# Kernel tuning notes

Measured on AMD Instinct MI355X. Metric: run time of the kernel, lower is better.

Reference implementation:

```python
import jax, jax.numpy as jnp
import numpy as np

N, E, NG = 8192, 65536, 8
EMB, SH = 32, 9
HID = EMB * SH
SDIM, M, KV = 16, 2048, 16  # M = master_rate*N masters (static top-k); KV virtual nbrs/node
RMAX, NB, PC = 10.0, 8, 5
MLPD, MSH, NL = 64, 32, 3
NEMB = 10


def _radial(r):
    # r: [E,1] -> Bessel basis * polynomial cutoff envelope, [E, NB]
    x = r / RMAX
    n = jnp.arange(1, NB + 1, dtype=r.dtype)
    bes = jnp.sqrt(2.0 / RMAX) * jnp.sin(n * jnp.pi * x) / jnp.maximum(r, 1e-9)
    p = float(PC)
    env = (1.0 - (p + 1) * (p + 2) / 2 * x ** PC + p * (p + 2) * x ** (PC + 1)
           - p * (p + 1) / 2 * x ** (PC + 2))
    env = jnp.where(x < 1.0, env, 0.0)
    return bes * env


def _sph(vec):
    # component-normalized real spherical harmonics l=0,1,2 of normalized vec
    r = jnp.linalg.norm(vec, axis=-1, keepdims=True)
    u = vec / jnp.maximum(r, 1e-9)
    x, y, z = u[..., 0], u[..., 1], u[..., 2]
    s3, s5, s15 = jnp.sqrt(3.0), jnp.sqrt(5.0), jnp.sqrt(15.0)
    Y = jnp.stack([
        jnp.ones_like(x),
        s3 * y, s3 * z, s3 * x,
        s15 * x * y, s15 * y * z, 0.5 * s5 * (3 * z * z - 1.0),
        s15 * x * z, 0.5 * s15 * (x * x - y * y)], axis=-1)
    return Y, r


def _conv(h, src, dst, sh, ef, W, rw1, rb1, rw2, rb2, valid, nnodes):
    # TFN-style conv: per-edge radial MLP -> per-sh-path weights, tensor product, scatter-sum
    rad = jax.nn.relu(ef @ rw1 + rb1) @ rw2 + rb2  # [E, SH]
    coeff = sh * rad                               # [E, SH]
    h_src = h[src]                                 # gather [E, in]
    out = W.shape[-1]
    msg = jnp.zeros((src.shape[0], out), h.dtype)
    for s in range(SH):  # small fixed loop over sh paths (avoids [E,in*SH] blowup)
        msg = msg + coeff[:, s:s + 1] * (h_src @ W[:, s, :])
    if valid is not None:
        msg = msg * valid[:, None]
    return jnp.zeros((nnodes, out), h.dtype).at[dst].add(msg)


def _scatter_softmax(sc, idx, nseg):
    mx = jax.ops.segment_max(sc, idx, nseg)
    e = jnp.exp(sc - mx[idx])
    s = jax.ops.segment_sum(e, idx, nseg)
    return e / (s[idx] + 1e-9)


def _forward(atoms, pos, edge_index, batch_ids, emb_table, W0, W12,
             rw1, rb1, rw2, rb2, msw1, msb1, msw2, msb2,
             vq, vk, aw1, ab1, aw2, ab2, pw1, pb1, pw2, pb2):
    h = emb_table[atoms]
    src, dst = edge_index[0], edge_index[1]
    for i in range(NL):
        W = W0 if i == 0 else W12[i - 1]
        # ---- local message passing over original edges ----
        vec = pos[src] - pos[dst]
        sh, r = _sph(vec)
        ef = _radial(r)
        h_up = _conv(h, src, dst, sh, ef, W, rw1[i], rb1[i], rw2[i], rb2[i], None, N)
        h_local = h_up.at[:, :h.shape[-1]].add(h)  # h_update + right-pad(h)
        # ---- master selection (static top-k of soft scores, k = master_rate*N) ----
        hs = h_local[:, :SDIM]
        m = jax.nn.sigmoid((jax.nn.relu(hs @ msw1[i] + msb1[i]) @ msw2[i] + msb2[i])[:, 0])
        _, midx = jax.lax.top_k(m, M)
        midx = jnp.sort(midx)
        inv = jnp.full((N,), -1, jnp.int32).at[midx].set(jnp.arange(M, dtype=jnp.int32))
        ms, md = inv[src], inv[dst]
        vi = (ms >= 0) & (md >= 0)           # induced-subgraph edge mask
        msc = jnp.where(vi, ms, 0)
        mdc = jnp.where(vi, md, 0)
        vif = vi.astype(h.dtype)
        h_m = h_local[midx]
        pos_m = pos[midx]
        hms = h_m[:, :SDIM]
        # induced dense adjacency over masters
        adj = jnp.minimum(jnp.zeros((M, M), h.dtype).at[msc, mdc].add(vif), 1.0)
        # ---- virtual edge generation (attention over masters) ----
        S = (hms @ vq[i]) @ (hms @ vk[i]).T / jnp.sqrt(jnp.asarray(SDIM, h.dtype))
        blocked = jnp.eye(M, dtype=bool) | (adj > 0)
        S = jnp.where(blocked, -jnp.inf, S)
        A_virtual = jax.nn.softmax(S, axis=-1)
        _, tk = jax.lax.top_k(S, KV)          # top-KV virtual nbrs per master (static)
        row = jnp.repeat(jnp.arange(M), KV)
        col = tk.reshape(-1)
        sv = jnp.concatenate([row, col])      # undirected virtual edges
        dv = jnp.concatenate([col, row])
        # ---- master-level edges: induced (masked) + virtual ----
        srcm = jnp.concatenate([msc, sv])
        dstm = jnp.concatenate([mdc, dv])
        vecm = pos_m[srcm] - pos_m[dstm]
        shm, rm = _sph(vecm)
        efm = _radial(rm)
        # scatter-softmax attention weights on virtual edges
        att_in = jnp.concatenate([hms[sv], hms[dv], efm[E:]], axis=-1)
        sc = (jax.nn.relu(att_in @ aw1[i] + ab1[i]) @ aw2[i] + ab2[i])[:, 0]
        wv = _scatter_softmax(sc, dv, M)
        full_w = jnp.concatenate([vif, wv])   # induced edges weight 1 (0 if invalid)
        efm = efm * full_w[:, None]
        if i == 0:
            h_hier = h_m  # first layer: in_irreps != out_irreps -> skip master conv
        else:
            validm = jnp.concatenate([vif, jnp.ones_like(wv)])
            h_mu = _conv(h_m, srcm, dstm, shm, efm, W,
                         rw1[i], rb1[i], rw2[i], rb2[i], validm, M)
            h_hier = h_mu + h_m
        # ---- scatter masters back, soft mix ----
        h_exp = jnp.zeros_like(h_local).at[midx].set(h_hier)
        me = m[:, None]
        h = (1.0 - me) * h_local + me * h_exp
    pooled = jax.ops.segment_sum(h[:, :EMB], batch_ids, NG)  # global_add_pool
    return jax.nn.relu(pooled @ pw1 + pb1) @ pw2 + pb2


def setup_inputs() -> dict:
    key = jax.random.key(0)
    ks = jax.random.split(key, 30)
    g = lambda k, shape, s=0.1: jax.random.normal(k, shape, jnp.float32) * s
    return dict(
        atoms=jax.random.randint(ks[0], (N,), 0, NEMB),
        pos=jax.random.normal(ks[1], (N, 3), jnp.float32) * 3.0,
        edge_index=jax.random.randint(ks[2], (2, E), 0, N),
        batch_ids=jnp.sort(jax.random.randint(ks[3], (N,), 0, NG)),
        emb_table=g(ks[4], (NEMB, EMB), 1.0),
        W0=g(ks[5], (EMB, SH, HID)),
        W12=g(ks[6], (NL - 1, HID, SH, HID), 0.05),
        rw1=g(ks[7], (NL, NB, MLPD), 0.3), rb1=g(ks[8], (NL, MLPD)),
        rw2=g(ks[9], (NL, MLPD, SH), 0.3), rb2=g(ks[10], (NL, SH)),
        msw1=g(ks[11], (NL, SDIM, MSH), 0.3), msb1=g(ks[12], (NL, MSH)),
        msw2=g(ks[13], (NL, MSH, 1), 0.3), msb2=g(ks[14], (NL, 1)),
        vq=g(ks[15], (NL, SDIM, SDIM), 0.3), vk=g(ks[16], (NL, SDIM, SDIM), 0.3),
        aw1=g(ks[17], (NL, 2 * SDIM + NB, SDIM), 0.3), ab1=g(ks[18], (NL, SDIM)),
        aw2=g(ks[19], (NL, SDIM, 1), 0.3), ab2=g(ks[20], (NL, 1)),
        pw1=g(ks[21], (EMB, EMB), 0.3), pb1=g(ks[22], (EMB,)),
        pw2=g(ks[23], (EMB, 1), 0.3), pb2=g(ks[24], (1,)),
    )


def reference(atoms, pos, edge_index, batch_ids, emb_table, W0, W12,
              rw1, rb1, rw2, rb2, msw1, msb1, msw2, msb2,
              vq, vk, aw1, ab1, aw2, ab2, pw1, pb1, pw2, pb2):
    return _forward(atoms, pos, edge_index, batch_ids, emb_table, W0, W12,
                    rw1, rb1, rw2, rb2, msw1, msb1, msw2, msb2,
                    vq, vk, aw1, ab1, aw2, ab2, pw1, pb1, pw2, pb2)
```

## Files before the change

### kernel.cpp

```cpp
#include <hip/hip_runtime.h>
#include <math.h>

#define NN     8192
#define EE     65536
#define NGR    8
#define EMBD   32
#define NSH    9
#define HIDD   288
#define SD     16
#define MM     2048
#define KVK    16
#define NBAS   8
#define MLPDIM 64
#define MSHD   32
#define MK     (MM*KVK)
#define EH     (EE + 2*MK)

typedef __attribute__((ext_vector_type(8))) short bf16x8;
typedef __attribute__((ext_vector_type(4))) float f32x4;

static __device__ __forceinline__ float relu_(float x) { return fmaxf(x, 0.f); }

__device__ __forceinline__ unsigned short f2b(float f) {
  unsigned int u = __float_as_uint(f);
  unsigned int r = (u + 0x7FFFu + ((u >> 16) & 1u)) >> 16;
  return (unsigned short)r;
}
__device__ __forceinline__ float b2f(unsigned short h) {
  return __uint_as_float(((unsigned int)h) << 16);
}

__device__ __forceinline__ void radial8(float r, float ef[8]) {
  float x = r * 0.1f;
  float invr = 1.0f / fmaxf(r, 1e-9f);
  float env = 0.0f;
  if (x < 1.0f) {
    float x2 = x * x, x4 = x2 * x2, x5 = x4 * x;
    env = 1.0f - 21.0f * x5 + 35.0f * x5 * x - 15.0f * x5 * x2;
  }
  const float cst = 0.4472135954999579f;
  float a = 3.14159265358979323846f * x;
#pragma unroll
  for (int n = 1; n <= NBAS; ++n)
    ef[n - 1] = cst * sinf((float)n * a) * invr * env;
}

__device__ __forceinline__ void sph9(float vx, float vy, float vz, float Y[9], float& r) {
  r = sqrtf(vx * vx + vy * vy + vz * vz);
  float inv = 1.0f / fmaxf(r, 1e-9f);
  float x = vx * inv, y = vy * inv, z = vz * inv;
  const float s3 = 1.7320508075688772f, s5 = 2.23606797749979f, s15 = 3.872983346207417f;
  Y[0] = 1.0f;
  Y[1] = s3 * y; Y[2] = s3 * z; Y[3] = s3 * x;
  Y[4] = s15 * x * y; Y[5] = s15 * y * z;
  Y[6] = 0.5f * s5 * (3.0f * z * z - 1.0f);
  Y[7] = s15 * x * z;
  Y[8] = 0.5f * s15 * (x * x - y * y);
}

__device__ __forceinline__ void radmlp(const float ef[8], const float* w1, const float* b1,
                                       const float* w2, const float* b2, float rad[9]) {
  float z[MLPDIM];
#pragma unroll
  for (int d = 0; d < MLPDIM; ++d) {
    float a = b1[d];
#pragma unroll
    for (int b = 0; b < NBAS; ++b) a += ef[b] * w1[b * MLPDIM + d];
    z[d] = relu_(a);
  }
#pragma unroll
  for (int s = 0; s < 9; ++s) {
    float a = b2[s];
#pragma unroll
    for (int d = 0; d < MLPDIM; ++d) a += z[d] * w2[d * 9 + s];
    rad[s] = a;
  }
}

__device__ __forceinline__ unsigned int fkey(float f) {
  unsigned int u = __float_as_uint(f);
  return (u & 0x80000000u) ? ~u : (u | 0x80000000u);
}
__device__ __forceinline__ float funkey(unsigned int k) {
  unsigned int u = (k & 0x80000000u) ? (k ^ 0x80000000u) : ~k;
  return __uint_as_float(u);
}

__device__ __forceinline__ void svdv(int j, const int* __restrict__ tkb, int& s, int& d) {
  if (j < MK) { s = j / KVK; d = tkb[j]; }
  else        { int t = j - MK; s = tkb[t]; d = t / KVK; }
}
__device__ __forceinline__ int dvof(int j, const int* __restrict__ tkb) {
  return (j < MK) ? tkb[j] : (j - MK) / KVK;
}


__global__ void k_init_h(const int* __restrict__ atoms, const float* __restrict__ emb,
                         float* __restrict__ hA) {
  int t = blockIdx.x * 256 + threadIdx.x;
  int n = t / HIDD, c = t - n * HIDD;
  hA[t] = (c < EMBD) ? emb[atoms[n] * EMBD + c] : 0.0f;
}

__global__ void k_geom(const float* __restrict__ pos, const int* __restrict__ ei,
                       float* __restrict__ sh_e, float* __restrict__ ef_e) {
  int e = blockIdx.x * 256 + threadIdx.x;
  int s = ei[e], d = ei[EE + e];
  float vx = pos[s * 3] - pos[d * 3];
  float vy = pos[s * 3 + 1] - pos[d * 3 + 1];
  float vz = pos[s * 3 + 2] - pos[d * 3 + 2];
  float Y[9], r;
  sph9(vx, vy, vz, Y, r);
  float ef[8]; radial8(r, ef);
#pragma unroll
  for (int t = 0; t < 9; ++t) sh_e[e * 9 + t] = Y[t];
#pragma unroll
  for (int b = 0; b < 8; ++b) ef_e[e * 8 + b] = ef[b];
}

__global__ __launch_bounds__(256) void k_radcoeff(const float* __restrict__ ef_e,
    const float* __restrict__ sh_e, const float* __restrict__ rw1, const float* __restrict__ rb1,
    const float* __restrict__ rw2, const float* __restrict__ rb2, float* __restrict__ coeff) {
  __shared__ float w1[NBAS * MLPDIM], b1[MLPDIM], w2[MLPDIM * 9], b2[9];
  int tid = threadIdx.x;
  for (int t = tid; t < NBAS * MLPDIM; t += 256) w1[t] = rw1[t];
  for (int t = tid; t < MLPDIM * 9; t += 256) w2[t] = rw2[t];
  if (tid < MLPDIM) b1[tid] = rb1[tid];
  if (tid < 9) b2[tid] = rb2[tid];
  __syncthreads();
  int e = blockIdx.x * 256 + tid;
  float ef[8];
#pragma unroll
  for (int b = 0; b < 8; ++b) ef[b] = ef_e[e * 8 + b];
  float rad[9]; radmlp(ef, w1, b1, w2, b2, rad);
#pragma unroll
  for (int s = 0; s < 9; ++s) coeff[(size_t)e * 9 + s] = sh_e[e * 9 + s] * rad[s];
}

__global__ __launch_bounds__(256) void k_wt(const float* __restrict__ W, int K,
                                            unsigned short* __restrict__ Whi,
                                            unsigned short* __restrict__ Wlo) {
  __shared__ unsigned short Th[32][290];
  __shared__ unsigned short Tl[32][290];
  int k0 = blockIdx.x * 32;
  int tid = threadIdx.x;
  for (int t = tid; t < 32 * 288; t += 256) {
    int kk = t / 288, o = t % 288;
    float wv = W[(size_t)(k0 + kk) * 288 + o];
    unsigned short hi = f2b(wv);
    Th[kk][o] = hi;
    Tl[kk][o] = f2b(wv - b2f(hi));
  }
  __syncthreads();
  for (int o = tid; o < 288; o += 256) {
    unsigned short th[32], tl[32];
#pragma unroll
    for (int kk = 0; kk < 32; ++kk) { th[kk] = Th[kk][o]; tl[kk] = Tl[kk][o]; }
#pragma unroll
    for (int q = 0; q < 4; ++q) {
      *(float4*)&Whi[(size_t)o * K + k0 + 8 * q] = *(float4*)&th[8 * q];
      *(float4*)&Wlo[(size_t)o * K + k0 + 8 * q] = *(float4*)&tl[8 * q];
    }
  }
}

__global__ void k_hist(const int* __restrict__ didx, int n, int* __restrict__ cnt) {
  int e = blockIdx.x * 256 + threadIdx.x;
  if (e >= n) return;
  int d = didx[e];
  if (d >= 0) atomicAdd(&cnt[d], 1);
}
__global__ __launch_bounds__(256) void k_scan(const int* __restrict__ cnt, int* __restrict__ off,
                                              int* __restrict__ cur, int nb) {
  __shared__ int ps[257];
  int tid = threadIdx.x;
  int chunk = nb / 256;
  int s = 0;
  for (int i = 0; i < chunk; ++i) s += cnt[tid * chunk + i];
  __shared__ int part[256];
  part[tid] = s;
  __syncthreads();
  if (tid == 0) {
    int a = 0;
    for (int i = 0; i < 256; ++i) { ps[i] = a; a += part[i]; }
    ps[256] = a;
  }
  __syncthreads();
  int a = ps[tid];
  for (int i = 0; i < chunk; ++i) {
    int idx = tid * chunk + i;
    off[idx] = a; cur[idx] = a;
    a += cnt[idx];
  }
  if (tid == 255) off[nb] = a;
}
__global__ void k_scat(const int* __restrict__ didx, int n, int* __restrict__ cur,
                       int* __restrict__ elist) {
  int e = blockIdx.x * 256 + threadIdx.x;
  if (e >= n) return;
  int d = didx[e];
  if (d < 0) return;
  int pos = atomicAdd(&cur[d], 1);
  elist[pos] = e;
}

template <int NJ>
__global__ __launch_bounds__(256) void k_gatherBbf(const float* __restrict__ h,
    const float* __restrict__ coeff, const int* __restrict__ sidx,
    const int* __restrict__ elist, const int* __restrict__ off,
    unsigned short* __restrict__ Ghi, unsigned short* __restrict__ Glo) {
  constexpr int INW = (NJ == 1) ? 32 : 288;
  constexpr int KG = INW * 9;
  __shared__ float red[3][64][NJ * 9];
  int w = threadIdx.x >> 6, l = threadIdx.x & 63;
  int d = blockIdx.x;
  int e0 = off[d], e1 = off[d + 1];
  float acc[NJ][9];
#pragma unroll
  for (int j = 0; j < NJ; ++j)
#pragma unroll
    for (int s = 0; s < 9; ++s) acc[j][s] = 0.f;
  for (int p = e0 + w; p < e1; p += 4) {
    int e = elist[p];
    int src = sidx[e];
    const float* hr = h + (size_t)src * HIDD;
    float hv[NJ];
#pragma unroll
    for (int j = 0; j < NJ; ++j)
      hv[j] = (l + 64 * j < INW) ? hr[l + 64 * j] : 0.f;
    const float* cfp = coeff + (size_t)e * 9;
    float cf[9];
#pragma unroll
    for (int s = 0; s < 9; ++s) cf[s] = cfp[s];
#pragma unroll
    for (int j = 0; j < NJ; ++j)
#pragma unroll
      for (int s = 0; s < 9; ++s) acc[j][s] += hv[j] * cf[s];
  }
  if (w > 0) {
#pragma unroll
    for (int j = 0; j < NJ; ++j)
#pragma unroll
      for (int s = 0; s < 9; ++s) red[w - 1][l][j * 9 + s] = acc[j][s];
  }
  __syncthreads();
  if (w == 0) {
    unsigned short* Gdh = Ghi + (size_t)d * KG;
    unsigned short* Gdl = Glo + (size_t)d * KG;
#pragma unroll
    for (int j = 0; j < NJ; ++j) {
      int k = l + 64 * j;
      if (k < INW) {
#pragma unroll
        for (int s = 0; s < 9; ++s) {
          float v = acc[j][s] + red[0][l][j * 9 + s] + red[1][l][j * 9 + s] +
                    red[2][l][j * 9 + s];
          unsigned short hi = f2b(v);
          Gdh[k * 9 + s] = hi;
          Gdl[k * 9 + s] = f2b(v - b2f(hi));
        }
      }
    }
  }
}

__global__ __launch_bounds__(256) void k_gatherBf(const float* __restrict__ h,
    const float* __restrict__ coeff, const int* __restrict__ sidx,
    const int* __restrict__ elist, const int* __restrict__ off, float* __restrict__ Gf) {
  constexpr int NJ = 5, INW = 288, KG = 2592, NW = 16;
  __shared__ float red[3][64][NJ * 9];
  int w = threadIdx.x >> 6, l = threadIdx.x & 63;
  int d = blockIdx.x, q = blockIdx.y;
  int e0 = off[d], e1 = off[d + 1];
  float acc[NJ][9];
#pragma unroll
  for (int j = 0; j < NJ; ++j)
#pragma unroll
    for (int s = 0; s < 9; ++s) acc[j][s] = 0.f;
  for (int p = e0 + q * 4 + w; p < e1; p += NW) {
    int e = elist[p];
    int src = sidx[e];
    const float* hr = h + (size_t)src * HIDD;
    float hv[NJ];
#pragma unroll
    for (int j = 0; j < NJ; ++j)
      hv[j] = (l + 64 * j < INW) ? hr[l + 64 * j] : 0.f;
    const float* cfp = coeff + (size_t)e * 9;
    float cf[9];
#pragma unroll
    for (int s = 0; s < 9; ++s) cf[s] = cfp[s];
#pragma unroll
    for (int j = 0; j < NJ; ++j)
#pragma unroll
      for (int s = 0; s < 9; ++s) acc[j][s] += hv[j] * cf[s];
  }
  if (w > 0) {
#pragma unroll
    for (int j = 0; j < NJ; ++j)
#pragma unroll
      for (int s = 0; s < 9; ++s) red[w - 1][l][j * 9 + s] = acc[j][s];
  }
  __syncthreads();
  if (w == 0) {
    float* Gd = Gf + ((size_t)q * gridDim.x + d) * KG;
#pragma unroll
    for (int j = 0; j < NJ; ++j) {
      int k = l + 64 * j;
      if (k < INW) {
#pragma unroll
        for (int s = 0; s < 9; ++s)
          Gd[k * 9 + s] = acc[j][s] + red[0][l][j * 9 + s] + red[1][l][j * 9 + s] +
                          red[2][l][j * 9 + s];
      }
    }
  }
}

__global__ void k_redG(const float* __restrict__ Gf, unsigned short* __restrict__ Ghi,
                       unsigned short* __restrict__ Glo) {
  const size_t PS = (size_t)MM * 2592;
  size_t t = (size_t)blockIdx.x * 256 + threadIdx.x;
  float v = Gf[t] + Gf[PS + t] + Gf[2 * PS + t] + Gf[3 * PS + t];
  unsigned short hi = f2b(v);
  Ghi[t] = hi;
  Glo[t] = f2b(v - b2f(hi));
}

template <int KK>
__global__ __launch_bounds__(256) void k_mgemm3(const unsigned short* __restrict__ Ahi,
    const unsigned short* __restrict__ Alo,
    const unsigned short* __restrict__ Whi, const unsigned short* __restrict__ Wlo,
    float* __restrict__ Cpart) {
  constexpr int slabs = KK / 32;
  __shared__ unsigned short Bh[144 * 40];
  __shared__ unsigned short Bl[144 * 40];
  int m0 = blockIdx.x * 64, cb = blockIdx.y * 144;
  int M = gridDim.x * 64;
  int Z = gridDim.z, z = blockIdx.z;
  int s0 = (z * slabs) / Z, s1 = ((z + 1) * slabs) / Z;
  float* C = Cpart + (size_t)z * M * 288;
  int tid = threadIdx.x;
  int w = tid >> 6, l = tid & 63;
  int lr = l & 15, oct = l >> 4;
  int arow = m0 + 16 * w + lr;
  f32x4 acc[9];
#pragma unroll
  for (int t = 0; t < 9; ++t) acc[t] = (f32x4){0.f, 0.f, 0.f, 0.f};
  for (int sl = s0; sl < s1; ++sl) {
    int k0 = sl * 32;
    __syncthreads();
    for (int t = tid; t < 1152; t += 256) {
      int hsel = t / 576;
      int qq = t - hsel * 576;
      int c = qq >> 2, ko = qq & 3;
      const unsigned short* Wsrc = hsel ? Wlo : Whi;
      float4 v = *(const float4*)&Wsrc[(size_t)(cb + c) * KK + k0 + ko * 8];
      unsigned short* Bdst = hsel ? Bl : Bh;
      *(float4*)&Bdst[c * 40 + ko * 8] = v;
    }
    __syncthreads();
    bf16x8 ah = *(const bf16x8*)&Ahi[(size_t)arow * KK + k0 + oct * 8];
    bf16x8 al = *(const bf16x8*)&Alo[(size_t)arow * KK + k0 + oct * 8];
#pragma unroll
    for (int t = 0; t < 9; ++t) {
      bf16x8 bh = *(const bf16x8*)&Bh[(16 * t + lr) * 40 + oct * 8];
      bf16x8 bl = *(const bf16x8*)&Bl[(16 * t + lr) * 40 + oct * 8];
      acc[t] = __builtin_amdgcn_mfma_f32_16x16x32_bf16(ah, bh, acc[t], 0, 0, 0);
      acc[t] = __builtin_amdgcn_mfma_f32_16x16x32_bf16(ah, bl, acc[t], 0, 0, 0);
      acc[t] = __builtin_amdgcn_mfma_f32_16x16x32_bf16(al, bh, acc[t], 0, 0, 0);
    }
  }
#pragma unroll
  for (int t = 0; t < 9; ++t) {
#pragma unroll
    for (int r = 0; r < 4; ++r)
      C[(size_t)(m0 + 16 * w + 4 * oct + r) * 288 + cb + 16 * t + lr] = acc[t][r];
  }
}

template <int Z>
__global__ void k_redN(const float* __restrict__ part, const float* __restrict__ hA,
                       float* __restrict__ hB, int INL) {
  int t = blockIdx.x * 256 + threadIdx.x;
  float v = 0.f;
#pragma unroll
  for (int z = 0; z < Z; ++z) v += part[(size_t)z * NN * 288 + t];
  int c = t % 288;
  if (c < INL) v += hA[t];
  hB[t] = v;
}
template <int Z>
__global__ void k_redH(const float* __restrict__ part, const float* __restrict__ hM,
                       float* __restrict__ hMu) {
  int t = blockIdx.x * 256 + threadIdx.x;
  float v = hM[t];
#pragma unroll
  for (int z = 0; z < Z; ++z) v += part[(size_t)z * MM * 288 + t];
  hMu[t] = v;
}

__global__ __launch_bounds__(256) void k_mmlp(const float* __restrict__ hB,
    const float* __restrict__ msw1, const float* __restrict__ msb1,
    const float* __restrict__ msw2, const float* __restrict__ msb2, float* __restrict__ mbuf) {
  __shared__ float w1[SD * MSHD], b1[MSHD], w2[MSHD];
  __shared__ float b2s;
  int tid = threadIdx.x;
  for (int t = tid; t < SD * MSHD; t += 256) w1[t] = msw1[t];
  if (tid < MSHD) { b1[tid] = msb1[tid]; w2[tid] = msw2[tid]; }
  if (tid == 0) b2s = msb2[0];
  __syncthreads();
  int n = blockIdx.x * 256 + tid;
  float hs[SD];
#pragma unroll
  for (int k = 0; k < SD; ++k) hs[k] = hB[(size_t)n * HIDD + k];
  float acc = b2s;
#pragma unroll
  for (int d = 0; d < MSHD; ++d) {
    float a = b1[d];
#pragma unroll
    for (int k = 0; k < SD; ++k) a += hs[k] * w1[k * MSHD + d];
    acc += relu_(a) * w2[d];
  }
  mbuf[n] = 1.0f / (1.0f + expf(-acc));
}

__global__ __launch_bounds__(256) void k_rank2(const float* __restrict__ mbuf,
                                               int* __restrict__ rankb) {
  __shared__ float vj[1024];
  __shared__ float vi_s[64];
  __shared__ int part[4][64];
  int tid = threadIdx.x;
  int i0 = blockIdx.x * 64, j0 = blockIdx.y * 1024;
  for (int t = tid; t < 1024; t += 256) vj[t] = mbuf[j0 + t];
  if (tid < 64) vi_s[tid] = mbuf[i0 + tid];
  __syncthreads();
  int il = tid & 63, js = tid >> 6;
  int i = i0 + il;
  float v = vi_s[il];
  int cnt = 0;
#pragma unroll 8
  for (int jj = js * 256; jj < js * 256 + 256; ++jj) {
    float w = vj[jj];
    cnt += (int)((w > v) | ((w == v) & (j0 + jj < i)));
  }
  part[js][il] = cnt;
  __syncthreads();
  if (tid < 64) {
    int c = part[0][tid] + part[1][tid] + part[2][tid] + part[3][tid];
    atomicAdd(&rankb[i0 + tid], c);
  }
}

__global__ __launch_bounds__(256) void k_select2(const int* __restrict__ rankb,
                                                 int* __restrict__ inv, int* __restrict__ midx) {
  __shared__ int part[256], ps[256];
  int tid = threadIdx.x;
  const int CH = NN / 256;
  int base = tid * CH;
  unsigned int mask = 0;
  int s = 0;
#pragma unroll
  for (int i = 0; i < CH; ++i) {
    int sel = (rankb[base + i] < MM) ? 1 : 0;
    mask |= (unsigned int)sel << i;
    s += sel;
  }
  part[tid] = s;
  __syncthreads();
  if (tid == 0) {
    int a = 0;
    for (int i = 0; i < 256; ++i) { ps[i] = a; a += part[i]; }
  }
  __syncthreads();
  int pos = ps[tid];
#pragma unroll
  for (int i = 0; i < CH; ++i) {
    if ((mask >> i) & 1u) {
      inv[base + i] = pos;
      midx[pos] = base + i;
      ++pos;
    } else {
      inv[base + i] = -1;
    }
  }
}

__global__ void k_gather_hm(const float* __restrict__ hB, const int* __restrict__ midx,
                            const float* __restrict__ pos, float* __restrict__ hM,
                            float* __restrict__ posm) {
  int t = blockIdx.x * 256 + threadIdx.x;
  int j = t / HIDD, c = t - j * HIDD;
  int n = midx[j];
  hM[t] = hB[(size_t)n * HIDD + c];
  if (c < 3) posm[j * 3 + c] = pos[n * 3 + c];
}

__global__ void k_qk(const float* __restrict__ hM, const float* __restrict__ vq,
                     const float* __restrict__ vk, float* __restrict__ qb, float* __restrict__ kb) {
  int g = blockIdx.x * 256 + threadIdx.x;
  int j = g >> 5, c = g & 31;
  const float* w = (c < 16) ? vq : vk;
  int cc = c & 15;
  float a = 0.f;
#pragma unroll
  for (int k = 0; k < SD; ++k) a += hM[(size_t)j * HIDD + k] * w[k * SD + cc];
  if (c < 16) qb[j * SD + cc] = a; else kb[j * SD + cc] = a;
}

__global__ __launch_bounds__(256) void k_S(const float* __restrict__ qb,
                                           const float* __restrict__ kb, float* __restrict__ S) {
  __shared__ float qs[64][17], ks[64][17];
  int r0 = blockIdx.y * 64, c0 = blockIdx.x * 64;
  int tid = threadIdx.x;
  for (int t = tid; t < 64 * 16; t += 256) {
    qs[t / 16][t % 16] = qb[(size_t)(r0 + t / 16) * SD + t % 16];
    ks[t / 16][t % 16] = kb[(size_t)(c0 + t / 16) * SD + t % 16];
  }
  __syncthreads();
  int tx = tid & 15, ty = tid >> 4;
  float acc[4][4] = {};
#pragma unroll
  for (int k = 0; k < 16; ++k) {
    float a[4], b[4];
#pragma unroll
    for (int i = 0; i < 4; ++i) a[i] = qs[ty * 4 + i][k];
#pragma unroll
    for (int j = 0; j < 4; ++j) b[j] = ks[tx * 4 + j][k];
#pragma unroll
    for (int i = 0; i < 4; ++i)
#pragma unroll
      for (int j = 0; j < 4; ++j) acc[i][j] += a[i] * b[j];
  }
#pragma unroll
  for (int i = 0; i < 4; ++i)
#pragma unroll
    for (int j = 0; j < 4; ++j) {
      int r = r0 + ty * 4 + i, c = c0 + tx * 4 + j;
      S[(size_t)r * MM + c] = (r == c) ? -INFINITY : acc[i][j] * 0.25f;
    }
}

__global__ void k_adj(const int* __restrict__ ei, const int* __restrict__ inv,
                      float* __restrict__ S) {
  int e = blockIdx.x * 256 + threadIdx.x;
  int ms = inv[ei[e]], md = inv[ei[EE + e]];
  if (ms >= 0 && md >= 0) S[(size_t)ms * MM + md] = -INFINITY;
}

__global__ __launch_bounds__(64) void k_topkv(const float* __restrict__ S, int* __restrict__ tkb) {
  int row = blockIdx.x;
  int lane = threadIdx.x;
  const float* Sr = S + (size_t)row * MM;
  float v[32];
#pragma unroll
  for (int t = 0; t < 32; ++t) v[t] = Sr[lane + 64 * t];
  unsigned int selmask = 0;
  for (int it = 0; it < KVK; ++it) {
    float best = -INFINITY;
    int bcol = 0x7fffffff;
#pragma unroll
    for (int t = 0; t < 32; ++t) {
      if (!((selmask >> t) & 1u)) {
        int c = lane + 64 * t;
        float val = v[t];
        if (val > best || (val == best && c < bcol)) { best = val; bcol = c; }
      }
    }
#pragma unroll
    for (int off = 1; off < 64; off <<= 1) {
      float ov = __shfl_xor(best, off);
      int oc = __shfl_xor(bcol, off);
      if (ov > best || (ov == best && oc < bcol)) { best = ov; bcol = oc; }
    }
    if (lane == (bcol & 63)) selmask |= 1u << (bcol >> 6);
    if (lane == 0) tkb[row * KVK + it] = bcol;
  }
}

__global__ __launch_bounds__(256) void k_att(const float* __restrict__ hM,
    const float* __restrict__ posm, const int* __restrict__ tkb,
    const float* __restrict__ aw1, const float* __restrict__ ab1,
    const float* __restrict__ aw2, const float* __restrict__ ab2, float* __restrict__ scb) {
  __shared__ float w1[40 * SD], b1[SD], w2[SD];
  __shared__ float b2s;
  int tid = threadIdx.x;
  for (int t = tid; t < 40 * SD; t += 256) w1[t] = aw1[t];
  if (tid < SD) { b1[tid] = ab1[tid]; w2[tid] = aw2[tid]; }
  if (tid == 0) b2s = ab2[0];
  __syncthreads();
  int j = blockIdx.x * 256 + tid;
  int s, d; svdv(j, tkb, s, d);
  float vx = posm[s * 3] - posm[d * 3];
  float vy = posm[s * 3 + 1] - posm[d * 3 + 1];
  float vz = posm[s * 3 + 2] - posm[d * 3 + 2];
  float r = sqrtf(vx * vx + vy * vy + vz * vz);
  float ef[8]; radial8(r, ef);
  float hsv[SD], hdv[SD];
#pragma unroll
  for (int k = 0; k < SD; ++k) { hsv[k] = hM[(size_t)s * HIDD + k]; hdv[k] = hM[(size_t)d * HIDD + k]; }
  float acc = b2s;
#pragma unroll
  for (int o = 0; o < SD; ++o) {
    float a = b1[o];
#pragma unroll
    for (int k = 0; k < SD; ++k) a += hsv[k] * w1[k * SD + o];
#pragma unroll
    for (int k = 0; k < SD; ++k) a += hdv[k] * w1[(SD + k) * SD + o];
#pragma unroll
    for (int b = 0; b < 8; ++b) a += ef[b] * w1[(2 * SD + b) * SD + o];
    acc += relu_(a) * w2[o];
  }
  scb[j] = acc;
}

__global__ void k_segmax(const float* __restrict__ scb, const int* __restrict__ tkb,
                         unsigned int* __restrict__ segmax) {
  int j = blockIdx.x * 256 + threadIdx.x;
  atomicMax(&segmax[dvof(j, tkb)], fkey(scb[j]));
}
__global__ void k_segexp(const float* __restrict__ scb, const int* __restrict__ tkb,
                         const unsigned int* __restrict__ segmax, float* __restrict__ segsum,
                         float* __restrict__ wvb) {
  int j = blockIdx.x * 256 + threadIdx.x;
  int d = dvof(j, tkb);
  float e = expf(scb[j] - funkey(segmax[d]));
  wvb[j] = e;
  atomicAdd(&segsum[d], e);
}

__global__ void k_hier_first(const int* __restrict__ ei, const int* __restrict__ inv,
                             int* __restrict__ sb, int* __restrict__ db) {
  int e = blockIdx.x * 256 + threadIdx.x;
  int ms = inv[ei[e]], md = inv[ei[EE + e]];
  bool val = (ms >= 0) && (md >= 0);
  sb[e] = val ? ms : 0;
  db[e] = val ? md : -1;
}

__global__ __launch_bounds__(256) void k_coeff_virt(const float* __restrict__ posm,
    const int* __restrict__ tkb, const float* __restrict__ wvb,
    const float* __restrict__ segsum,
    const float* __restrict__ rw1, const float* __restrict__ rb1,
    const float* __restrict__ rw2, const float* __restrict__ rb2,
    float* __restrict__ coeff, int* __restrict__ sb, int* __restrict__ db) {
  __shared__ float w1[NBAS * MLPDIM], b1[MLPDIM], w2[MLPDIM * 9], b2[9];
  int tid = threadIdx.x;
  for (int t = tid; t < NBAS * MLPDIM; t += 256) w1[t] = rw1[t];
  for (int t = tid; t < MLPDIM * 9; t += 256) w2[t] = rw2[t];
  if (tid < MLPDIM) b1[tid] = rb1[tid];
  if (tid < 9) b2[tid] = rb2[tid];
  __syncthreads();
  int j = blockIdx.x * 256 + tid;
  int s, d; svdv(j, tkb, s, d);
  float vx = posm[s * 3] - posm[d * 3];
  float vy = posm[s * 3 + 1] - posm[d * 3 + 1];
  float vz = posm[s * 3 + 2] - posm[d * 3 + 2];
  float Y[9], r;
  sph9(vx, vy, vz, Y, r);
  float ef[8]; radial8(r, ef);
  float w = wvb[j] / (segsum[d] + 1e-9f);
#pragma unroll
  for (int b = 0; b < 8; ++b) ef[b] *= w;
  float rad[9]; radmlp(ef, w1, b1, w2, b2, rad);
  int e = EE + j;
#pragma unroll
  for (int t = 0; t < 9; ++t) coeff[(size_t)e * 9 + t] = Y[t] * rad[t];
  sb[e] = s;
  db[e] = d;
}

__global__ void k_combine(const float* __restrict__ hB, const float* __restrict__ hier,
                          const float* __restrict__ mbuf, const int* __restrict__ inv,
                          float* __restrict__ hA) {
  int t = blockIdx.x * 256 + threadIdx.x;
  int n = t / HIDD;
  float f = mbuf[n];
  float v = (1.0f - f) * hB[t];
  int j = inv[n];
  if (j >= 0) v += f * hier[(size_t)j * HIDD + (t - n * HIDD)];
  hA[t] = v;
}

__global__ void k_pool(const float* __restrict__ hA, const int* __restrict__ bids,
                       float* __restrict__ pooled) {
  int t = blockIdx.x * 256 + threadIdx.x;
  int n = t / EMBD, c = t - n * EMBD;
  atomicAdd(&pooled[bids[n] * EMBD + c], hA[(size_t)n * HIDD + c]);
}

__global__ void k_head(const float* __restrict__ pooled, const float* __restrict__ pw1,
                       const float* __restrict__ pb1, const float* __restrict__ pw2,
                       const float* __restrict__ pb2, float* __restrict__ out) {
  __shared__ float z[NGR][EMBD];
  int tid = threadIdx.x;
  int g = tid / EMBD, c2 = tid % EMBD;
  if (g < NGR) {
    float a = pb1[c2];
    for (int c = 0; c < EMBD; ++c) a += pooled[g * EMBD + c] * pw1[c * EMBD + c2];
    z[g][c2] = relu_(a);
  }
  __syncthreads();
  if (tid < NGR) {
    float a = pb2[0];
    for (int c = 0; c < EMBD; ++c) a += z[tid][c] * pw2[c];
    out[tid] = a;
  }
}


extern "C" void kernel_launch(void* const* d_in, const int* in_sizes, int n_in,
                              void* d_out, int out_size, void* d_ws, size_t ws_size,
                              hipStream_t stream) {
  const int* atoms = (const int*)d_in[0];
  const float* pos = (const float*)d_in[1];
  const int* ei = (const int*)d_in[2];
  const int* bids = (const int*)d_in[3];
  const float* emb = (const float*)d_in[4];
  const float* W0 = (const float*)d_in[5];
  const float* W12 = (const float*)d_in[6];
  const float* rw1 = (const float*)d_in[7];
  const float* rb1 = (const float*)d_in[8];
  const float* rw2 = (const float*)d_in[9];
  const float* rb2 = (const float*)d_in[10];
  const float* msw1 = (const float*)d_in[11];
  const float* msb1 = (const float*)d_in[12];
  const float* msw2 = (const float*)d_in[13];
  const float* msb2 = (const float*)d_in[14];
  const float* vq = (const float*)d_in[15];
  const float* vk = (const float*)d_in[16];
  const float* aw1 = (const float*)d_in[17];
  const float* ab1 = (const float*)d_in[18];
  const float* aw2 = (const float*)d_in[19];
  const float* ab2 = (const float*)d_in[20];
  const float* pw1 = (const float*)d_in[21];
  const float* pb1 = (const float*)d_in[22];
  const float* pw2 = (const float*)d_in[23];
  const float* pb2 = (const float*)d_in[24];
  float* out = (float*)d_out;

  char* p = (char*)d_ws;
  auto alloc = [&](size_t n) { char* r = p; p += (n + 255) & ~(size_t)255; return r; };
  float* hA = (float*)alloc((size_t)NN * HIDD * 4);
  float* hB = (float*)alloc((size_t)NN * HIDD * 4);
  float* hM = (float*)alloc((size_t)MM * HIDD * 4);
  float* hMu = (float*)alloc((size_t)MM * HIDD * 4);
  float* S = (float*)alloc((size_t)MM * MM * 4);
  float* sh_e = (float*)alloc((size_t)EE * 9 * 4);
  float* ef_e = (float*)alloc((size_t)EE * 8 * 4);
  float* coeff = (float*)alloc((size_t)EH * 9 * 4);
  float* mbuf = (float*)alloc((size_t)NN * 4);
  int* rankb = (int*)alloc((size_t)NN * 4);
  int* inv = (int*)alloc((size_t)NN * 4);
  int* midx = (int*)alloc((size_t)MM * 4);
  float* posm = (float*)alloc((size_t)MM * 3 * 4);
  float* qb = (float*)alloc((size_t)MM * SD * 4);
  float* kb = (float*)alloc((size_t)MM * SD * 4);
  int* tkb = (int*)alloc((size_t)MM * KVK * 4);
  float* scb = (float*)alloc((size_t)2 * MK * 4);
  float* wvb = (float*)alloc((size_t)2 * MK * 4);
  unsigned int* segmax = (unsigned int*)alloc((size_t)MM * 4);
  float* segsum = (float*)alloc((size_t)MM * 4);
  int* sb = (int*)alloc((size_t)EH * 4);
  int* db = (int*)alloc((size_t)EH * 4);
  float* pooled = (float*)alloc((size_t)NGR * EMBD * 4);
  char* Gblk = alloc((size_t)NN * 2592 * 4);
  unsigned short* Ghi = (unsigned short*)Gblk;
  unsigned short* Glo = Ghi + (size_t)NN * 2592;
  float* Gf = (float*)Gblk;
  unsigned short* Ghhi = (unsigned short*)alloc((size_t)MM * 2592 * 2);
  unsigned short* Ghlo = (unsigned short*)alloc((size_t)MM * 2592 * 2);
  unsigned short* Wh0 = (unsigned short*)alloc((size_t)288 * 288 * 2);
  unsigned short* Wl0 = (unsigned short*)alloc((size_t)288 * 288 * 2);
  unsigned short* Wh1 = (unsigned short*)alloc((size_t)2592 * 288 * 2);
  unsigned short* Wl1 = (unsigned short*)alloc((size_t)2592 * 288 * 2);
  unsigned short* Wh2 = (unsigned short*)alloc((size_t)2592 * 288 * 2);
  unsigned short* Wl2 = (unsigned short*)alloc((size_t)2592 * 288 * 2);
  float* Cpart = (float*)alloc((size_t)4 * NN * 288 * 4);
  int* cntN = (int*)alloc((size_t)NN * 4);
  int* offN = (int*)alloc((size_t)(NN + 1) * 4);
  int* curN = (int*)alloc((size_t)NN * 4);
  int* elN = (int*)alloc((size_t)EE * 4);
  int* cntH = (int*)alloc((size_t)MM * 4);
  int* offH = (int*)alloc((size_t)(MM + 1) * 4);
  int* curH = (int*)alloc((size_t)MM * 4);
  int* elH = (int*)alloc((size_t)EH * 4);

  const int* srcI = ei;
  const int* dstI = ei + EE;

  k_init_h<<<NN * HIDD / 256, 256, 0, stream>>>(atoms, emb, hA);
  k_geom<<<EE / 256, 256, 0, stream>>>(pos, ei, sh_e, ef_e);

  k_wt<<<288 / 32, 256, 0, stream>>>(W0, 288, Wh0, Wl0);
  k_wt<<<2592 / 32, 256, 0, stream>>>(W12, 2592, Wh1, Wl1);
  k_wt<<<2592 / 32, 256, 0, stream>>>(W12 + (size_t)2592 * 288, 2592, Wh2, Wl2);

  hipMemsetAsync(cntN, 0, NN * 4, stream);
  k_hist<<<EE / 256, 256, 0, stream>>>(dstI, EE, cntN);
  k_scan<<<1, 256, 0, stream>>>(cntN, offN, curN, NN);
  k_scat<<<EE / 256, 256, 0, stream>>>(dstI, EE, curN, elN);

  for (int L = 0; L < 3; ++L) {
    const unsigned short* Wh = (L == 0) ? Wh0 : ((L == 1) ? Wh1 : Wh2);
    const unsigned short* Wl = (L == 0) ? Wl0 : ((L == 1) ? Wl1 : Wl2);
    const float* lrw1 = rw1 + L * NBAS * MLPDIM;
    const float* lrb1 = rb1 + L * MLPDIM;
    const float* lrw2 = rw2 + L * MLPDIM * 9;
    const float* lrb2 = rb2 + L * 9;

    k_radcoeff<<<EE / 256, 256, 0, stream>>>(ef_e, sh_e, lrw1, lrb1, lrw2, lrb2, coeff);
    if (L == 0) {
      k_gatherBbf<1><<<NN, 256, 0, stream>>>(hA, coeff, srcI, elN, offN, Ghi, Glo);
      k_mgemm3<288><<<dim3(NN / 64, 2, 2), 256, 0, stream>>>(Ghi, Glo, Wh, Wl, Cpart);
      k_redN<2><<<NN * 288 / 256, 256, 0, stream>>>(Cpart, hA, hB, EMBD);
    } else {
      k_gatherBbf<5><<<NN, 256, 0, stream>>>(hA, coeff, srcI, elN, offN, Ghi, Glo);
      k_mgemm3<2592><<<dim3(NN / 64, 2, 4), 256, 0, stream>>>(Ghi, Glo, Wh, Wl, Cpart);
      k_redN<4><<<NN * 288 / 256, 256, 0, stream>>>(Cpart, hA, hB, HIDD);
    }
    k_mmlp<<<NN / 256, 256, 0, stream>>>(hB, msw1 + L * SD * MSHD, msb1 + L * MSHD,
                                         msw2 + L * MSHD, msb2 + L, mbuf);
    hipMemsetAsync(rankb, 0, NN * 4, stream);
    k_rank2<<<dim3(NN / 64, 8), 256, 0, stream>>>(mbuf, rankb);
    k_select2<<<1, 256, 0, stream>>>(rankb, inv, midx);
    k_gather_hm<<<MM * HIDD / 256, 256, 0, stream>>>(hB, midx, pos, hM, posm);

    if (L > 0) {
      k_qk<<<MM * 32 / 256, 256, 0, stream>>>(hM, vq + L * SD * SD, vk + L * SD * SD, qb, kb);
      k_S<<<dim3(MM / 64, MM / 64), 256, 0, stream>>>(qb, kb, S);
      k_adj<<<EE / 256, 256, 0, stream>>>(ei, inv, S);
      k_topkv<<<MM, 64, 0, stream>>>(S, tkb);
      k_att<<<2 * MK / 256, 256, 0, stream>>>(hM, posm, tkb, aw1 + L * 40 * SD, ab1 + L * SD,
                                              aw2 + L * SD, ab2 + L, scb);
      hipMemsetAsync(segmax, 0, MM * 4, stream);
      hipMemsetAsync(segsum, 0, MM * 4, stream);
      k_segmax<<<2 * MK / 256, 256, 0, stream>>>(scb, tkb, segmax);
      k_segexp<<<2 * MK / 256, 256, 0, stream>>>(scb, tkb, segmax, segsum, wvb);
      k_hier_first<<<EE / 256, 256, 0, stream>>>(ei, inv, sb, db);
      k_coeff_virt<<<2 * MK / 256, 256, 0, stream>>>(posm, tkb, wvb, segsum,
                                                     lrw1, lrb1, lrw2, lrb2, coeff, sb, db);
      hipMemsetAsync(cntH, 0, MM * 4, stream);
      k_hist<<<EH / 256, 256, 0, stream>>>(db, EH, cntH);
      k_scan<<<1, 256, 0, stream>>>(cntH, offH, curH, MM);
      k_scat<<<EH / 256, 256, 0, stream>>>(db, EH, curH, elH);
      k_gatherBf<<<dim3(MM, 4), 256, 0, stream>>>(hM, coeff, sb, elH, offH, Gf);
      k_redG<<<MM * 2592 / 256, 256, 0, stream>>>(Gf, Ghhi, Ghlo);
      k_mgemm3<2592><<<dim3(MM / 64, 2, 8), 256, 0, stream>>>(Ghhi, Ghlo, Wh, Wl, Cpart);
      k_redH<8><<<MM * 288 / 256, 256, 0, stream>>>(Cpart, hM, hMu);
    }
    const float* hier = (L == 0) ? hM : hMu;
    k_combine<<<NN * HIDD / 256, 256, 0, stream>>>(hB, hier, mbuf, inv, hA);
  }

  hipMemsetAsync(pooled, 0, (size_t)NGR * EMBD * 4, stream);
  k_pool<<<NN * EMBD / 256, 256, 0, stream>>>(hA, bids, pooled);
  k_head<<<1, 256, 0, stream>>>(pooled, pw1, pb1, pw2, pb2, out);
}
```

Before: 1.290 ms.

## Precompute sorted edge sources, coalesce gather writeback, drop rank atomics and memsets

Edge scatter now also writes each sorted edge's source index. The gather kernels read it directly instead of chasing elist then sidx, and they process two edges per iteration. Gather results are first reduced into shared memory, then written by all 256 threads in a contiguous, coalesced pattern instead of strided writes from a single wave. Ranking writes per-slice partial counts to an 8x buffer that select sums, which removes the atomics and the memset. The attention kernel loads node features as float4, and the two segment memsets are merged into one, which assumes segmax and segsum sit next to each other in memory.

```diff
diff --git a/kernel.cpp b/kernel.cpp
--- a/kernel.cpp
+++ b/kernel.cpp
@@ -194,20 +194,21 @@
   }
   if (tid == 255) off[nb] = a;
 }
-__global__ void k_scat(const int* __restrict__ didx, int n, int* __restrict__ cur,
-                       int* __restrict__ elist) {
+__global__ void k_scat(const int* __restrict__ didx, const int* __restrict__ sidx, int n,
+                       int* __restrict__ cur, int* __restrict__ elist, int* __restrict__ esrc) {
   int e = blockIdx.x * 256 + threadIdx.x;
   if (e >= n) return;
   int d = didx[e];
   if (d < 0) return;
   int pos = atomicAdd(&cur[d], 1);
   elist[pos] = e;
+  esrc[pos] = sidx[e];
 }
 
 template <int NJ>
 __global__ __launch_bounds__(256) void k_gatherBbf(const float* __restrict__ h,
-    const float* __restrict__ coeff, const int* __restrict__ sidx,
-    const int* __restrict__ elist, const int* __restrict__ off,
+    const float* __restrict__ coeff, const int* __restrict__ elist,
+    const int* __restrict__ esrc, const int* __restrict__ off,
     unsigned short* __restrict__ Ghi, unsigned short* __restrict__ Glo) {
   constexpr int INW = (NJ == 1) ? 32 : 288;
   constexpr int KG = INW * 9;
@@ -220,9 +221,9 @@
   for (int j = 0; j < NJ; ++j)
 #pragma unroll
     for (int s = 0; s < 9; ++s) acc[j][s] = 0.f;
-  for (int p = e0 + w; p < e1; p += 4) {
+  auto edge = [&](int p) {
     int e = elist[p];
-    int src = sidx[e];
+    int src = esrc[p];
     const float* hr = h + (size_t)src * HIDD;
     float hv[NJ];
 #pragma unroll
@@ -236,7 +237,10 @@
     for (int j = 0; j < NJ; ++j)
 #pragma unroll
       for (int s = 0; s < 9; ++s) acc[j][s] += hv[j] * cf[s];
-  }
+  };
+  int p = e0 + w;
+  for (; p + 4 < e1; p += 8) { edge(p); edge(p + 4); }
+  if (p < e1) edge(p);
   if (w > 0) {
 #pragma unroll
     for (int j = 0; j < NJ; ++j)
@@ -245,28 +249,29 @@
   }
   __syncthreads();
   if (w == 0) {
-    unsigned short* Gdh = Ghi + (size_t)d * KG;
-    unsigned short* Gdl = Glo + (size_t)d * KG;
-#pragma unroll
-    for (int j = 0; j < NJ; ++j) {
-      int k = l + 64 * j;
-      if (k < INW) {
-#pragma unroll
-        for (int s = 0; s < 9; ++s) {
-          float v = acc[j][s] + red[0][l][j * 9 + s] + red[1][l][j * 9 + s] +
-                    red[2][l][j * 9 + s];
-          unsigned short hi = f2b(v);
-          Gdh[k * 9 + s] = hi;
-          Gdl[k * 9 + s] = f2b(v - b2f(hi));
-        }
+#pragma unroll
+    for (int j = 0; j < NJ; ++j)
+#pragma unroll
+      for (int s = 0; s < 9; ++s) {
+        int idx = j * 9 + s;
+        red[0][l][idx] = acc[j][s] + red[0][l][idx] + red[1][l][idx] + red[2][l][idx];
       }
-    }
+  }
+  __syncthreads();
+  unsigned short* Gdh = Ghi + (size_t)d * KG;
+  unsigned short* Gdl = Glo + (size_t)d * KG;
+  for (int i = threadIdx.x; i < KG; i += 256) {
+    int k = i / 9, s = i - 9 * k;
+    float v = red[0][k & 63][(k >> 6) * 9 + s];
+    unsigned short hi = f2b(v);
+    Gdh[i] = hi;
+    Gdl[i] = f2b(v - b2f(hi));
   }
 }
 
 __global__ __launch_bounds__(256) void k_gatherBf(const float* __restrict__ h,
-    const float* __restrict__ coeff, const int* __restrict__ sidx,
-    const int* __restrict__ elist, const int* __restrict__ off, float* __restrict__ Gf) {
+    const float* __restrict__ coeff, const int* __restrict__ elist,
+    const int* __restrict__ esrc, const int* __restrict__ off, float* __restrict__ Gf) {
   constexpr int NJ = 5, INW = 288, KG = 2592, NW = 16;
   __shared__ float red[3][64][NJ * 9];
   int w = threadIdx.x >> 6, l = threadIdx.x & 63;
@@ -277,14 +282,15 @@
   for (int j = 0; j < NJ; ++j)
 #pragma unroll
     for (int s = 0; s < 9; ++s) acc[j][s] = 0.f;
-  for (int p = e0 + q * 4 + w; p < e1; p += NW) {
+  auto edge = [&](int p) {
     int e = elist[p];
-    int src = sidx[e];
+    int src = esrc[p];
     const float* hr = h + (size_t)src * HIDD;
     float hv[NJ];
 #pragma unroll
     for (int j = 0; j < NJ; ++j)
-      hv[j] = (l + 64 * j < INW) ? hr[l + 64 * j] : 0.f;
+      hv[j] = hr[l + 64 * j < INW ? l + 64 * j : 0];
+    if (l + 256 >= INW) hv[4] = 0.f;
     const float* cfp = coeff + (size_t)e * 9;
     float cf[9];
 #pragma unroll
@@ -293,7 +299,10 @@
     for (int j = 0; j < NJ; ++j)
 #pragma unroll
       for (int s = 0; s < 9; ++s) acc[j][s] += hv[j] * cf[s];
-  }
+  };
+  int p = e0 + q * 4 + w;
+  for (; p + NW < e1; p += 2 * NW) { edge(p); edge(p + NW); }
+  if (p < e1) edge(p);
   if (w > 0) {
 #pragma unroll
     for (int j = 0; j < NJ; ++j)
@@ -302,17 +311,19 @@
   }
   __syncthreads();
   if (w == 0) {
-    float* Gd = Gf + ((size_t)q * gridDim.x + d) * KG;
-#pragma unroll
-    for (int j = 0; j < NJ; ++j) {
-      int k = l + 64 * j;
-      if (k < INW) {
-#pragma unroll
-        for (int s = 0; s < 9; ++s)
-          Gd[k * 9 + s] = acc[j][s] + red[0][l][j * 9 + s] + red[1][l][j * 9 + s] +
-                          red[2][l][j * 9 + s];
+#pragma unroll
+    for (int j = 0; j < NJ; ++j)
+#pragma unroll
+      for (int s = 0; s < 9; ++s) {
+        int idx = j * 9 + s;
+        red[0][l][idx] = acc[j][s] + red[0][l][idx] + red[1][l][idx] + red[2][l][idx];
       }
-    }
+  }
+  __syncthreads();
+  float* Gd = Gf + ((size_t)q * gridDim.x + d) * KG;
+  for (int i = threadIdx.x; i < KG; i += 256) {
+    int k = i / 9, s = i - 9 * k;
+    Gd[i] = red[0][k & 63][(k >> 6) * 9 + s];
   }
 }
 
@@ -425,7 +436,7 @@
 }
 
 __global__ __launch_bounds__(256) void k_rank2(const float* __restrict__ mbuf,
-                                               int* __restrict__ rankb) {
+                                               int* __restrict__ rank8) {
   __shared__ float vj[1024];
   __shared__ float vi_s[64];
   __shared__ int part[4][64];
@@ -447,11 +458,11 @@
   __syncthreads();
   if (tid < 64) {
     int c = part[0][tid] + part[1][tid] + part[2][tid] + part[3][tid];
-    atomicAdd(&rankb[i0 + tid], c);
-  }
-}
-
-__global__ __launch_bounds__(256) void k_select2(const int* __restrict__ rankb,
+    rank8[(size_t)blockIdx.y * NN + i0 + tid] = c;
+  }
+}
+
+__global__ __launch_bounds__(256) void k_select2(const int* __restrict__ rank8,
                                                  int* __restrict__ inv, int* __restrict__ midx) {
   __shared__ int part[256], ps[256];
   int tid = threadIdx.x;
@@ -461,7 +472,10 @@
   int s = 0;
 #pragma unroll
   for (int i = 0; i < CH; ++i) {
-    int sel = (rankb[base + i] < MM) ? 1 : 0;
+    int r = 0;
+#pragma unroll
+    for (int y = 0; y < 8; ++y) r += rank8[(size_t)y * NN + base + i];
+    int sel = (r < MM) ? 1 : 0;
     mask |= (unsigned int)sel << i;
     s += sel;
   }
@@ -596,8 +610,16 @@
   float r = sqrtf(vx * vx + vy * vy + vz * vz);
   float ef[8]; radial8(r, ef);
   float hsv[SD], hdv[SD];
-#pragma unroll
-  for (int k = 0; k < SD; ++k) { hsv[k] = hM[(size_t)s * HIDD + k]; hdv[k] = hM[(size_t)d * HIDD + k]; }
+  {
+    const float4* ps4 = (const float4*)&hM[(size_t)s * HIDD];
+    const float4* pd4 = (const float4*)&hM[(size_t)d * HIDD];
+#pragma unroll
+    for (int q = 0; q < 4; ++q) {
+      float4 a = ps4[q], b = pd4[q];
+      hsv[4 * q] = a.x; hsv[4 * q + 1] = a.y; hsv[4 * q + 2] = a.z; hsv[4 * q + 3] = a.w;
+      hdv[4 * q] = b.x; hdv[4 * q + 1] = b.y; hdv[4 * q + 2] = b.z; hdv[4 * q + 3] = b.w;
+    }
+  }
   float acc = b2s;
 #pragma unroll
   for (int o = 0; o < SD; ++o) {
@@ -749,7 +771,7 @@
   float* ef_e = (float*)alloc((size_t)EE * 8 * 4);
   float* coeff = (float*)alloc((size_t)EH * 9 * 4);
   float* mbuf = (float*)alloc((size_t)NN * 4);
-  int* rankb = (int*)alloc((size_t)NN * 4);
+  int* rank8 = (int*)alloc((size_t)8 * NN * 4);
   int* inv = (int*)alloc((size_t)NN * 4);
   int* midx = (int*)alloc((size_t)MM * 4);
   float* posm = (float*)alloc((size_t)MM * 3 * 4);
@@ -780,10 +802,12 @@
   int* offN = (int*)alloc((size_t)(NN + 1) * 4);
   int* curN = (int*)alloc((size_t)NN * 4);
   int* elN = (int*)alloc((size_t)EE * 4);
+  int* esrcN = (int*)alloc((size_t)EE * 4);
   int* cntH = (int*)alloc((size_t)MM * 4);
   int* offH = (int*)alloc((size_t)(MM + 1) * 4);
   int* curH = (int*)alloc((size_t)MM * 4);
   int* elH = (int*)alloc((size_t)EH * 4);
+  int* esrcH = (int*)alloc((size_t)EH * 4);
 
   const int* srcI = ei;
   const int* dstI = ei + EE;
@@ -798,7 +822,7 @@
   hipMemsetAsync(cntN, 0, NN * 4, stream);
   k_hist<<<EE / 256, 256, 0, stream>>>(dstI, EE, cntN);
   k_scan<<<1, 256, 0, stream>>>(cntN, offN, curN, NN);
-  k_scat<<<EE / 256, 256, 0, stream>>>(dstI, EE, curN, elN);
+  k_scat<<<EE / 256, 256, 0, stream>>>(dstI, srcI, EE, curN, elN, esrcN);
 
   for (int L = 0; L < 3; ++L) {
     const unsigned short* Wh = (L == 0) ? Wh0 : ((L == 1) ? Wh1 : Wh2);
@@ -810,19 +834,18 @@
 
     k_radcoeff<<<EE / 256, 256, 0, stream>>>(ef_e, sh_e, lrw1, lrb1, lrw2, lrb2, coeff);
     if (L == 0) {
-      k_gatherBbf<1><<<NN, 256, 0, stream>>>(hA, coeff, srcI, elN, offN, Ghi, Glo);
+      k_gatherBbf<1><<<NN, 256, 0, stream>>>(hA, coeff, elN, esrcN, offN, Ghi, Glo);
       k_mgemm3<288><<<dim3(NN / 64, 2, 2), 256, 0, stream>>>(Ghi, Glo, Wh, Wl, Cpart);
       k_redN<2><<<NN * 288 / 256, 256, 0, stream>>>(Cpart, hA, hB, EMBD);
     } else {
-      k_gatherBbf<5><<<NN, 256, 0, stream>>>(hA, coeff, srcI, elN, offN, Ghi, Glo);
+      k_gatherBbf<5><<<NN, 256, 0, stream>>>(hA, coeff, elN, esrcN, offN, Ghi, Glo);
       k_mgemm3<2592><<<dim3(NN / 64, 2, 4), 256, 0, stream>>>(Ghi, Glo, Wh, Wl, Cpart);
       k_redN<4><<<NN * 288 / 256, 256, 0, stream>>>(Cpart, hA, hB, HIDD);
     }
     k_mmlp<<<NN / 256, 256, 0, stream>>>(hB, msw1 + L * SD * MSHD, msb1 + L * MSHD,
                                          msw2 + L * MSHD, msb2 + L, mbuf);
-    hipMemsetAsync(rankb, 0, NN * 4, stream);
-    k_rank2<<<dim3(NN / 64, 8), 256, 0, stream>>>(mbuf, rankb);
-    k_select2<<<1, 256, 0, stream>>>(rankb, inv, midx);
+    k_rank2<<<dim3(NN / 64, 8), 256, 0, stream>>>(mbuf, rank8);
+    k_select2<<<1, 256, 0, stream>>>(rank8, inv, midx);
     k_gather_hm<<<MM * HIDD / 256, 256, 0, stream>>>(hB, midx, pos, hM, posm);
 
     if (L > 0) {
@@ -832,8 +855,7 @@
       k_topkv<<<MM, 64, 0, stream>>>(S, tkb);
       k_att<<<2 * MK / 256, 256, 0, stream>>>(hM, posm, tkb, aw1 + L * 40 * SD, ab1 + L * SD,
                                               aw2 + L * SD, ab2 + L, scb);
-      hipMemsetAsync(segmax, 0, MM * 4, stream);
-      hipMemsetAsync(segsum, 0, MM * 4, stream);
+      hipMemsetAsync(segmax, 0, 2 * MM * 4, stream);
       k_segmax<<<2 * MK / 256, 256, 0, stream>>>(scb, tkb, segmax);
       k_segexp<<<2 * MK / 256, 256, 0, stream>>>(scb, tkb, segmax, segsum, wvb);
       k_hier_first<<<EE / 256, 256, 0, stream>>>(ei, inv, sb, db);
@@ -842,8 +864,8 @@
       hipMemsetAsync(cntH, 0, MM * 4, stream);
       k_hist<<<EH / 256, 256, 0, stream>>>(db, EH, cntH);
       k_scan<<<1, 256, 0, stream>>>(cntH, offH, curH, MM);
-      k_scat<<<EH / 256, 256, 0, stream>>>(db, EH, curH, elH);
-      k_gatherBf<<<dim3(MM, 4), 256, 0, stream>>>(hM, coeff, sb, elH, offH, Gf);
+      k_scat<<<EH / 256, 256, 0, stream>>>(db, sb, EH, curH, elH, esrcH);
+      k_gatherBf<<<dim3(MM, 4), 256, 0, stream>>>(hM, coeff, elH, esrcH, offH, Gf);
       k_redG<<<MM * 2592 / 256, 256, 0, stream>>>(Gf, Ghhi, Ghlo);
       k_mgemm3<2592><<<dim3(MM / 64, 2, 8), 256, 0, stream>>>(Ghhi, Ghlo, Wh, Wl, Cpart);
       k_redH<8><<<MM * 288 / 256, 256, 0, stream>>>(Cpart, hM, hMu);
```

After: 1.274 ms. About the same (-1.2%).
